# Optimization experiments

Hardware: AMD Instinct MI355X
Metric: run time of the kernel (lower is better)

The kernel has to match this reference:

```python
import jax, jax.numpy as jnp
import numpy as np

SHIFT_SIZE = 5
PAD = SHIFT_SIZE // 2  # 2
MAX_SHIFT = 2


def conv3x3(x, w, b):
    # x: [B,Cin,H,W], w: [Cout,Cin,3,3]
    y = jax.lax.conv_general_dilated(
        x, w, window_strides=(1, 1), padding='SAME',
        dimension_numbers=('NCHW', 'OIHW', 'NCHW'))
    return y + b[None, :, None, None]


def shift_groups(xn, shifts, axis):
    # xn: [B,C,Hp,Wp]; roll each of the SHIFT_SIZE channel groups by its own shift along `axis`
    B, C, Hp, Wp = xn.shape
    G = shifts.shape[0]
    Cg = C // G
    xg = xn.reshape(B, G, Cg, Hp, Wp)
    rolled = jax.vmap(lambda xc, s: jnp.roll(xc, s, axis=axis),
                      in_axes=(1, 0), out_axes=1)(xg, shifts)  # xc: [B,Cg,Hp,Wp]
    return rolled.reshape(B, C, Hp, Wp)


def setup_inputs() -> dict:
    key = jax.random.key(0)
    ks = jax.random.split(key, 8)
    B, C, H, W = 16, 320, 64, 64
    x = jax.random.normal(ks[0], (B, C, H, W), dtype=jnp.float32)
    edge_guidance = jax.random.normal(ks[1], (B, C, H, W), dtype=jnp.float32)
    w1 = jax.random.normal(ks[2], (16, 1, 3, 3), dtype=jnp.float32) * 0.2
    b1 = jnp.zeros((16,), dtype=jnp.float32)
    w2 = jax.random.normal(ks[3], (2, 16, 3, 3), dtype=jnp.float32) * 0.2
    b2 = jnp.zeros((2,), dtype=jnp.float32)
    shifts_h = jax.random.randint(ks[4], (SHIFT_SIZE,), -MAX_SHIFT, MAX_SHIFT + 1, dtype=jnp.int32)
    shifts_w = jax.random.randint(ks[5], (SHIFT_SIZE,), -MAX_SHIFT, MAX_SHIFT + 1, dtype=jnp.int32)
    return {'x': x, 'edge_guidance': edge_guidance, 'w1': w1, 'b1': b1,
            'w2': w2, 'b2': b2, 'shifts_h': shifts_h, 'shifts_w': shifts_w}


def reference(x, edge_guidance, w1, b1, w2, b2, shifts_h, shifts_w):
    B, C, H, W = x.shape
    # zero-pad spatial dims by PAD on each side
    xn = jnp.pad(x, ((0, 0), (0, 0), (PAD, PAD), (PAD, PAD)))
    # direction gating from edge guidance
    edge_map = jnp.mean(edge_guidance, axis=1, keepdims=True)  # [B,1,H,W]
    h = jax.nn.relu(conv3x3(edge_map, w1, b1))
    dir_logits = conv3x3(h, w2, b2)                            # [B,2,H,W]
    dir_weights = jax.nn.softmax(dir_logits, axis=1)
    # channel-grouped rolls along H and along W, then crop back
    shifted_h = shift_groups(xn, shifts_h, axis=2)[:, :, PAD:PAD + H, PAD:PAD + W]
    shifted_w = shift_groups(xn, shifts_w, axis=3)[:, :, PAD:PAD + H, PAD:PAD + W]
    x_shift = dir_weights[:, 0:1] * shifted_h + dir_weights[:, 1:2] * shifted_w
    return x_shift
```

## Files before the change

kernel.cpp:

```cpp
#include <hip/hip_runtime.h>

#define BATCH 16
#define CHAN  320
#define HH    64
#define WW    64
#define PLANE (HH*WW)
#define NGRP  5
#define CG    64
#define CPB   4

__device__ float g_em[BATCH * PLANE];
__device__ float g_w0[BATCH * PLANE];

__global__ void k_reduce_mean(const float* __restrict__ eg)
{
    __shared__ float red[256];
    const int bid = blockIdx.x;
    const int b = bid >> 6;
    const int r = bid & 63;
    const int q   = threadIdx.x & 63;
    const int grp = threadIdx.x >> 6;

    const float* p = eg + (((size_t)b * CHAN + (size_t)grp * 80) * PLANE) + r * WW + q;
    float s = 0.f;
#pragma unroll 8
    for (int c = 0; c < 80; ++c)
        s += p[(size_t)c * PLANE];

    red[threadIdx.x] = s;
    __syncthreads();
    if (grp == 0) {
        g_em[(size_t)bid * 64 + q] = red[q] + red[q + 64] + red[q + 128] + red[q + 192];
    }
}

__global__ void k_conv_dir(const float* __restrict__ w1, const float* __restrict__ b1,
                           const float* __restrict__ w2, const float* __restrict__ b2)
{
    __shared__ float sem[20][20];
    __shared__ float shh[18][18];
    __shared__ float sw1[16][9];
    __shared__ float sb1[16];
    __shared__ float sw2[2][16][9];
    __shared__ float sb2[2];

    const int bid = blockIdx.x;
    const int b  = bid >> 4;
    const int t  = bid & 15;
    const int r0 = (t >> 2) * 16;
    const int q0 = (t & 3) * 16;
    const int tid = threadIdx.x;

    if (tid < 144) sw1[tid / 9][tid % 9] = w1[tid];
    if (tid < 16)  sb1[tid] = b1[tid];
    for (int i = tid; i < 288; i += 256) ((float*)sw2)[i] = w2[i];
    if (tid < 2)   sb2[tid] = b2[tid];

    const float scale = 1.0f / (float)CHAN;
    for (int i = tid; i < 400; i += 256) {
        const int lr = i / 20, lq = i % 20;
        const int r = r0 + lr - 2, q = q0 + lq - 2;
        float v = 0.f;
        if ((unsigned)r < HH && (unsigned)q < WW)
            v = g_em[((size_t)b * HH + r) * WW + q] * scale;
        sem[lr][lq] = v;
    }
    __syncthreads();

    const int lr = tid >> 4;
    const int lq = tid & 15;
    float l0 = sb2[0];
    float l1 = sb2[1];

    for (int i = 0; i < 16; ++i) {
        for (int p = tid; p < 324; p += 256) {
            const int hr = p / 18, hq = p % 18;
            const int gr = r0 - 1 + hr, gq = q0 - 1 + hq;
            float acc = 0.f;
            if ((unsigned)gr < HH && (unsigned)gq < WW) {
                acc = sb1[i];
#pragma unroll
                for (int dr = 0; dr < 3; ++dr)
#pragma unroll
                    for (int dq = 0; dq < 3; ++dq)
                        acc += sem[hr + dr][hq + dq] * sw1[i][dr * 3 + dq];
                acc = fmaxf(acc, 0.f);
            }
            shh[hr][hq] = acc;
        }
        __syncthreads();
#pragma unroll
        for (int dr = 0; dr < 3; ++dr)
#pragma unroll
            for (int dq = 0; dq < 3; ++dq) {
                const float hv = shh[lr + dr][lq + dq];
                l0 += hv * sw2[0][i][dr * 3 + dq];
                l1 += hv * sw2[1][i][dr * 3 + dq];
            }
        __syncthreads();
    }

    const float m  = fmaxf(l0, l1);
    const float e0 = expf(l0 - m);
    const float e1 = expf(l1 - m);
    const float w0v = e0 / (e0 + e1);
    g_w0[((size_t)b * HH + (r0 + lr)) * WW + (q0 + lq)] = w0v;
}

__global__ void k_shift_blend(const float* __restrict__ x,
                              const int* __restrict__ sh_arr, const int* __restrict__ sw_arr,
                              float* __restrict__ out)
{
    const int bid = blockIdx.x;
    const int nb  = CHAN / CPB;
    const int cb  = bid % nb;
    const int b   = bid / nb;
    const int c0  = cb * CPB;
    const int g   = c0 >> 6;
    const int sh  = sh_arr[g];
    const int sw  = sw_arr[g];

    const float* wp = g_w0 + (size_t)b * PLANE;

    float4 wv[4];
#pragma unroll
    for (int j = 0; j < 4; ++j)
        wv[j] = ((const float4*)wp)[threadIdx.x + j * 256];

#pragma unroll
    for (int cc = 0; cc < CPB; ++cc) {
        const float* xp = x   + ((size_t)b * CHAN + c0 + cc) * PLANE;
        float*       op = out + ((size_t)b * CHAN + c0 + cc) * PLANE;

#pragma unroll
        for (int j = 0; j < 4; ++j) {
            const int p4 = threadIdx.x + j * 256;
            const int r  = p4 >> 4;
            const int q4 = p4 & 15;
            const int q  = q4 * 4;
            const int base = r * WW + q;

            const float4 xv = ((const float4*)xp)[p4];

            float4 xh = make_float4(0.f, 0.f, 0.f, 0.f);
            const int rs = r - sh;
            if ((unsigned)rs < HH)
                xh = *(const float4*)(xp + rs * WW + q);

            float xw0, xw1, xw2, xw3;
            if (sw == 0) {
                xw0 = xv.x; xw1 = xv.y; xw2 = xv.z; xw3 = xv.w;
            } else if (sw > 0) {
                int off = base - 4; if (off < 0) off = 0;
                const float4 xm = *(const float4*)(xp + off);
                if (sw == 1) { xw0 = xm.w; xw1 = xv.x; xw2 = xv.y; xw3 = xv.z; }
                else         { xw0 = xm.z; xw1 = xm.w; xw2 = xv.x; xw3 = xv.y; }
                if (q == 0) { xw0 = 0.f; if (sw == 2) xw1 = 0.f; }
            } else {
                int off = base + 4; if (off > PLANE - 4) off = PLANE - 4;
                const float4 xr = *(const float4*)(xp + off);
                if (sw == -1) { xw0 = xv.y; xw1 = xv.z; xw2 = xv.w; xw3 = xr.x; }
                else          { xw0 = xv.z; xw1 = xv.w; xw2 = xr.x; xw3 = xr.y; }
                if (q == WW - 4) { xw3 = 0.f; if (sw == -2) xw2 = 0.f; }
            }

            float4 o;
            o.x = xw0 + wv[j].x * (xh.x - xw0);
            o.y = xw1 + wv[j].y * (xh.y - xw1);
            o.z = xw2 + wv[j].z * (xh.z - xw2);
            o.w = xw3 + wv[j].w * (xh.w - xw3);
            ((float4*)op)[p4] = o;
        }
    }
}

extern "C" void kernel_launch(void* const* d_in, const int* in_sizes, int n_in,
                              void* d_out, int out_size, void* d_ws, size_t ws_size,
                              hipStream_t stream)
{
    const float* x   = (const float*)d_in[0];
    const float* eg  = (const float*)d_in[1];
    const float* w1  = (const float*)d_in[2];
    const float* b1  = (const float*)d_in[3];
    const float* w2  = (const float*)d_in[4];
    const float* b2  = (const float*)d_in[5];
    const int*   shh = (const int*)d_in[6];
    const int*   shw = (const int*)d_in[7];
    float* out = (float*)d_out;

    k_reduce_mean<<<BATCH * HH, 256, 0, stream>>>(eg);
    k_conv_dir<<<BATCH * 16, 256, 0, stream>>>(w1, b1, w2, b2);
    k_shift_blend<<<BATCH * (CHAN / CPB), 256, 0, stream>>>(x, shh, shw, out);
}
```

Measured before the change: 59.27 us.

## Stage shift-blend input planes in LDS via direct global-to-LDS loads

The shift-blend kernel now copies each block's channel planes into shared memory with global_load_lds DMA, then does the shifted neighbour reads from LDS instead of global memory. Channels per block drop from 4 to 2 so the 32KB staging buffer fits, and output stores become nontemporal. This targets the redundant global and cache traffic from the overlapping shifted reads. In exchange it adds shared-memory pressure that limits occupancy, a full-block barrier, and more blocks.

```diff
diff --git a/kernel.cpp b/kernel.cpp
--- a/kernel.cpp
+++ b/kernel.cpp
@@ -7,7 +7,9 @@
 #define PLANE (HH*WW)
 #define NGRP  5
 #define CG    64
-#define CPB   4
+#define CPB   2
+
+typedef float vfloat4 __attribute__((ext_vector_type(4)));
 
 __device__ float g_em[BATCH * PLANE];
 __device__ float g_w0[BATCH * PLANE];
@@ -107,10 +109,17 @@
     g_w0[((size_t)b * HH + (r0 + lr)) * WW + (q0 + lq)] = w0v;
 }
 
-__global__ void k_shift_blend(const float* __restrict__ x,
-                              const int* __restrict__ sh_arr, const int* __restrict__ sw_arr,
-                              float* __restrict__ out)
-{
+__global__ __launch_bounds__(256) void k_shift_blend(
+        const float* __restrict__ x,
+        const int* __restrict__ sh_arr, const int* __restrict__ sw_arr,
+        float* __restrict__ out)
+{
+    __shared__ float sx[CPB * PLANE];
+
+    const int tid  = threadIdx.x;
+    const int lane = tid & 63;
+    const int wave = tid >> 6;
+
     const int bid = blockIdx.x;
     const int nb  = CHAN / CPB;
     const int cb  = bid % nb;
@@ -120,56 +129,67 @@
     const int sh  = sh_arr[g];
     const int sw  = sw_arr[g];
 
+    const char* gbase = (const char*)(x + ((size_t)b * CHAN + c0) * PLANE);
+#pragma unroll
+    for (int i = 0; i < 8; ++i) {
+        const int byte_off = (wave * 8 + i) * 1024 + lane * 16;
+        __builtin_amdgcn_global_load_lds(
+            (const __attribute__((address_space(1))) unsigned int*)(gbase + byte_off),
+            (__attribute__((address_space(3))) unsigned int*)((char*)sx + (wave * 8 + i) * 1024),
+            16, 0, 0);
+    }
+
     const float* wp = g_w0 + (size_t)b * PLANE;
-
     float4 wv[4];
 #pragma unroll
     for (int j = 0; j < 4; ++j)
-        wv[j] = ((const float4*)wp)[threadIdx.x + j * 256];
+        wv[j] = ((const float4*)wp)[tid + j * 256];
+
+    __syncthreads();
 
 #pragma unroll
     for (int cc = 0; cc < CPB; ++cc) {
-        const float* xp = x   + ((size_t)b * CHAN + c0 + cc) * PLANE;
-        float*       op = out + ((size_t)b * CHAN + c0 + cc) * PLANE;
+        float* op = out + ((size_t)b * CHAN + c0 + cc) * PLANE;
+        const float* sp = sx + cc * PLANE;
 
 #pragma unroll
         for (int j = 0; j < 4; ++j) {
-            const int p4 = threadIdx.x + j * 256;
+            const int p4 = tid + j * 256;
             const int r  = p4 >> 4;
             const int q4 = p4 & 15;
             const int q  = q4 * 4;
             const int base = r * WW + q;
 
-            const float4 xv = ((const float4*)xp)[p4];
+            const float4 xv = *(const float4*)(sp + base);
 
             float4 xh = make_float4(0.f, 0.f, 0.f, 0.f);
             const int rs = r - sh;
             if ((unsigned)rs < HH)
-                xh = *(const float4*)(xp + rs * WW + q);
+                xh = *(const float4*)(sp + rs * WW + q);
 
             float xw0, xw1, xw2, xw3;
             if (sw == 0) {
                 xw0 = xv.x; xw1 = xv.y; xw2 = xv.z; xw3 = xv.w;
             } else if (sw > 0) {
                 int off = base - 4; if (off < 0) off = 0;
-                const float4 xm = *(const float4*)(xp + off);
+                const float4 xm = *(const float4*)(sp + off);
                 if (sw == 1) { xw0 = xm.w; xw1 = xv.x; xw2 = xv.y; xw3 = xv.z; }
                 else         { xw0 = xm.z; xw1 = xm.w; xw2 = xv.x; xw3 = xv.y; }
                 if (q == 0) { xw0 = 0.f; if (sw == 2) xw1 = 0.f; }
             } else {
                 int off = base + 4; if (off > PLANE - 4) off = PLANE - 4;
-                const float4 xr = *(const float4*)(xp + off);
+                const float4 xr = *(const float4*)(sp + off);
                 if (sw == -1) { xw0 = xv.y; xw1 = xv.z; xw2 = xv.w; xw3 = xr.x; }
                 else          { xw0 = xv.z; xw1 = xv.w; xw2 = xr.x; xw3 = xr.y; }
                 if (q == WW - 4) { xw3 = 0.f; if (sw == -2) xw2 = 0.f; }
             }
 
-            float4 o;
+            vfloat4 o;
             o.x = xw0 + wv[j].x * (xh.x - xw0);
             o.y = xw1 + wv[j].y * (xh.y - xw1);
             o.z = xw2 + wv[j].z * (xh.z - xw2);
             o.w = xw3 + wv[j].w * (xh.w - xw3);
-            ((float4*)op)[p4] = o;
+            __builtin_nontemporal_store(o, (vfloat4*)op + p4);
         }
     }
 }
```

After: 58.02 us. -2.1%, faster.
